# Optimization experiments

Measured on AMD Instinct MI355X. Metric: run time of the kernel, lower is better.

Reference implementation:

```python
import jax, jax.numpy as jnp
import numpy as np

D_MODEL = 1024
D_STATE = 16
EXPAND = 2
D_HEAD = 64
D_CONV = 4
FFN = 2816
NORMALIZE_BC = True
D_INNER = EXPAND * D_MODEL          # 2048
N_HEADS = D_INNER // D_HEAD         # 32
EPS = 1e-6


def _rmsnorm(x, w):
    v = jnp.mean(x * x, axis=-1, keepdims=True)
    return x * jax.lax.rsqrt(v + EPS) * w


def _mixer(x, in_proj_w, conv_w, conv_b, A_log, dt_bias, D, out_proj_w):
    b, l, _ = x.shape
    zxbcdt = x @ in_proj_w.T  # (b, l, 2*D_INNER + 2*D_STATE + N_HEADS)
    z, xBC, dt_raw = jnp.split(zxbcdt, [D_INNER, 2 * D_INNER + 2 * D_STATE], axis=-1)
    # causal depthwise conv over (u, B, C) channels
    xp = jnp.pad(xBC, ((0, 0), (D_CONV - 1, 0), (0, 0)))
    y = conv_b + sum(xp[:, k:k + l, :] * conv_w[:, k] for k in range(D_CONV))
    xBC = jax.nn.silu(y)
    u, Bm, Cm = jnp.split(xBC, [D_INNER, D_INNER + D_STATE], axis=-1)
    if NORMALIZE_BC:
        Bm = Bm / (jnp.linalg.norm(Bm, axis=-1, keepdims=True) + EPS)
        Cm = Cm / (jnp.linalg.norm(Cm, axis=-1, keepdims=True) + EPS)
    dt = jax.nn.softplus(dt_raw + dt_bias)          # (b, l, h)
    A = jnp.exp(A_log)                              # (h, n) oscillator frequencies >= 0
    u = u.reshape(b, l, N_HEADS, D_HEAD)

    # LinOSS implicit (IM) discretization of z' = -A y + B u ; y' = z
    #   S  = 1/(1 + dt^2 A)
    #   w_k = S*(w_{k-1} - dt*A*y_{k-1} + dt*B u_k)
    #   y_k = y_{k-1} + dt*w_k ;  out_k = C y_k + D u_k
    def step(carry, inp):
        w, ys = carry                               # each (b, h, dh, n)
        dt_t, B_t, C_t, u_t = inp                   # (b,h),(b,n),(b,n),(b,h,dh)
        S = 1.0 / (1.0 + (dt_t[:, :, None] ** 2) * A[None])   # (b,h,n)
        Sb = S[:, :, None, :]
        dtb = dt_t[:, :, None, None]
        Ab = A[None, :, None, :]
        Bu = B_t[:, None, None, :] * u_t[..., None]            # (b,h,dh,n)
        w = Sb * (w - dtb * Ab * ys + dtb * Bu)
        ys = ys + dtb * w
        o = jnp.einsum('bhdn,bn->bhd', ys, C_t)
        return (w, ys), o

    init = (jnp.zeros((b, N_HEADS, D_HEAD, D_STATE), x.dtype),
            jnp.zeros((b, N_HEADS, D_HEAD, D_STATE), x.dtype))
    xs = (dt.transpose(1, 0, 2), Bm.transpose(1, 0, 2),
          Cm.transpose(1, 0, 2), u.transpose(1, 0, 2, 3))
    _, ys = jax.lax.scan(step, init, xs)            # (l, b, h, dh)
    ys = ys.transpose(1, 0, 2, 3) + D[None, None, :, None] * u
    out = ys.reshape(b, l, D_INNER) * jax.nn.silu(z)
    return out @ out_proj_w.T


def setup_inputs() -> dict:
    key = jax.random.key(0)
    ks = jax.random.split(key, 12)
    B, L = 4, 2048
    proj_dim = 2 * D_INNER + 2 * D_STATE + N_HEADS
    conv_ch = D_INNER + 2 * D_STATE
    s = lambda k, shape, sc: jax.random.normal(k, shape, jnp.float32) * sc
    return {
        "x": s(ks[0], (B, L, D_MODEL), 1.0),
        "norm1_w": jnp.ones((D_MODEL,), jnp.float32),
        "in_proj_w": s(ks[1], (proj_dim, D_MODEL), D_MODEL ** -0.5),
        "conv_w": s(ks[2], (conv_ch, D_CONV), 0.3),
        "conv_b": jnp.zeros((conv_ch,), jnp.float32),
        "A_log": s(ks[3], (N_HEADS, D_STATE), 0.5),
        "dt_bias": s(ks[4], (N_HEADS,), 0.5),
        "D": s(ks[5], (N_HEADS,), 1.0),
        "out_proj_w": s(ks[6], (D_MODEL, D_INNER), D_INNER ** -0.5),
        "norm2_w": jnp.ones((D_MODEL,), jnp.float32),
        "gate_w": s(ks[7], (FFN, D_MODEL), D_MODEL ** -0.5),
        "up_w": s(ks[8], (FFN, D_MODEL), D_MODEL ** -0.5),
        "down_w": s(ks[9], (D_MODEL, FFN), FFN ** -0.5),
    }


def reference(x, norm1_w, in_proj_w, conv_w, conv_b, A_log, dt_bias, D,
              out_proj_w, norm2_w, gate_w, up_w, down_w):
    h = x + _mixer(_rmsnorm(x, norm1_w), in_proj_w, conv_w, conv_b,
                   A_log, dt_bias, D, out_proj_w)
    hn = _rmsnorm(h, norm2_w)
    ffn = (jax.nn.silu(hn @ gate_w.T) * (hn @ up_w.T)) @ down_w.T
    return h + ffn
```

## Files before the change

kernel.cpp:

```cpp
#include <hip/hip_runtime.h>
#include <hip/hip_bf16.h>

#define D_MODEL   1024
#define D_STATE   16
#define D_HEAD    64
#define D_CONV    4
#define FFN_DIM   2816
#define D_INNER   2048
#define N_HEADS   32
#define BATCH     4
#define SEQ       2048
#define ROWS      (BATCH*SEQ)
#define PROJ_DIM  4160
#define PROJ_PAD  4352
#define CONV_CH   2080
#define CH        128
#define NCH       (SEQ/CH)

typedef __bf16 bf16x8 __attribute__((ext_vector_type(8)));
typedef float  f32x4  __attribute__((ext_vector_type(4)));
typedef float  f32x2  __attribute__((ext_vector_type(2)));

__device__ __forceinline__ float siluf(float x) { return x / (1.0f + __expf(-x)); }

#define SBAR() do { asm volatile("" ::: "memory"); __builtin_amdgcn_s_barrier(); asm volatile("" ::: "memory"); } while (0)
#define LGKM0() asm volatile("s_waitcnt lgkmcnt(0)" ::: "memory")
#define VMCNT4() asm volatile("s_waitcnt vmcnt(4)" ::: "memory")
#define VMCNT2() asm volatile("s_waitcnt vmcnt(2)" ::: "memory")
#define VMCNT0() asm volatile("s_waitcnt vmcnt(0)" ::: "memory")

__global__ void cvt_k(const float* __restrict__ src, __hip_bfloat16* __restrict__ dst, int n) {
  int i = blockIdx.x * blockDim.x + threadIdx.x;
  if (i < n) dst[i] = __float2bfloat16(src[i]);
}

__global__ void cvt_pad_k(const float* __restrict__ src, __hip_bfloat16* __restrict__ dst) {
  int i = blockIdx.x * blockDim.x + threadIdx.x;
  if (i >= PROJ_PAD * D_MODEL) return;
  int row = i >> 10;
  dst[i] = (row < PROJ_DIM) ? __float2bfloat16(src[i]) : __float2bfloat16(0.0f);
}

__global__ __launch_bounds__(256) void rmsnorm_k(const float* __restrict__ x,
                                                 const float* __restrict__ w,
                                                 __hip_bfloat16* __restrict__ out,
                                                 float* __restrict__ outf) {
  int row = blockIdx.x;
  int t = threadIdx.x;
  const float* xr = x + (size_t)row * D_MODEL;
  float4 v = ((const float4*)xr)[t];
  float ss = v.x*v.x + v.y*v.y + v.z*v.z + v.w*v.w;
  #pragma unroll
  for (int o = 32; o > 0; o >>= 1) ss += __shfl_xor(ss, o);
  __shared__ float red[4];
  if ((t & 63) == 0) red[t >> 6] = ss;
  __syncthreads();
  ss = red[0] + red[1] + red[2] + red[3];
  float scale = rsqrtf(ss * (1.0f / D_MODEL) + 1e-6f);
  float4 wv = ((const float4*)w)[t];
  float4 r;
  r.x = v.x * scale * wv.x; r.y = v.y * scale * wv.y;
  r.z = v.z * scale * wv.z; r.w = v.w * scale * wv.w;
  __hip_bfloat16* orow = out + (size_t)row * D_MODEL + t * 4;
  orow[0] = __float2bfloat16(r.x);
  orow[1] = __float2bfloat16(r.y);
  orow[2] = __float2bfloat16(r.z);
  orow[3] = __float2bfloat16(r.w);
  if (outf) ((float4*)(outf + (size_t)row * D_MODEL))[t] = r;
}

__global__ __launch_bounds__(256) void dtproj_k(const float* __restrict__ xn,
                                                const float* __restrict__ wi,
                                                const float* __restrict__ dtb,
                                                float* __restrict__ dtT) {
  const int r0 = blockIdx.x * 4;
  const int t  = threadIdx.x;
  const int hh  = t >> 3;
  const int seg = t & 7;

  __shared__ float xs[4][D_MODEL];
  #pragma unroll
  for (int i = 0; i < 4; ++i)
    ((float4*)&xs[i][0])[t] = ((const float4*)(xn + (size_t)(r0 + i) * D_MODEL))[t];
  __syncthreads();

  const float4* w4 = (const float4*)(wi + (size_t)(2 * D_INNER + 2 * D_STATE + hh) * D_MODEL) + seg * 32;
  const float4* x0 = (const float4*)&xs[0][0] + seg * 32;
  const float4* x1 = (const float4*)&xs[1][0] + seg * 32;
  const float4* x2 = (const float4*)&xs[2][0] + seg * 32;
  const float4* x3 = (const float4*)&xs[3][0] + seg * 32;
  float a0 = 0.f, a1 = 0.f, a2 = 0.f, a3 = 0.f;
  #pragma unroll 8
  for (int k = 0; k < 32; ++k) {
    float4 wv = w4[k];
    float4 v0 = x0[k], v1 = x1[k], v2 = x2[k], v3 = x3[k];
    a0 = fmaf(wv.x, v0.x, fmaf(wv.y, v0.y, fmaf(wv.z, v0.z, fmaf(wv.w, v0.w, a0))));
    a1 = fmaf(wv.x, v1.x, fmaf(wv.y, v1.y, fmaf(wv.z, v1.z, fmaf(wv.w, v1.w, a1))));
    a2 = fmaf(wv.x, v2.x, fmaf(wv.y, v2.y, fmaf(wv.z, v2.z, fmaf(wv.w, v2.w, a2))));
    a3 = fmaf(wv.x, v3.x, fmaf(wv.y, v3.y, fmaf(wv.z, v3.z, fmaf(wv.w, v3.w, a3))));
  }
  #pragma unroll
  for (int m = 1; m < 8; m <<= 1) {
    a0 += __shfl_xor(a0, m);
    a1 += __shfl_xor(a1, m);
    a2 += __shfl_xor(a2, m);
    a3 += __shfl_xor(a3, m);
  }
  if (seg == 0) {
    float bias = dtb[hh];
    float v[4] = {a0, a1, a2, a3};
    #pragma unroll
    for (int i = 0; i < 4; ++i) {
      float xv = v[i] + bias;
      dtT[(size_t)hh * ROWS + r0 + i] = (xv > 20.f) ? xv : log1pf(__expf(xv));
    }
  }
}

template<int EPI>
__global__ __launch_bounds__(512, 2) void gemm8(
    const __hip_bfloat16* __restrict__ A,
    const __hip_bfloat16* __restrict__ Bw,
    float* __restrict__ Cf,
    __hip_bfloat16* __restrict__ Cb,
    const float* __restrict__ add_src,
    int M, int N, int K)
{
  extern __shared__ char lds[];
  const int nwg = (M >> 8) * (N >> 8);
  int bid = blockIdx.x;
  bid = (bid & 7) * (nwg >> 3) + (bid >> 3);
  const int ntn = N >> 8;
  const int bm = (bid / ntn) << 8;
  const int bn = (bid % ntn) << 8;

  const int tid  = threadIdx.x;
  const int wid  = tid >> 6;
  const int lane = tid & 63;
  const int wm = wid >> 2;
  const int wn = wid & 3;
  const int r16 = lane & 15;
  const int kg  = lane >> 4;

  const int rb = ((r16 << 6) + (kg << 4)) ^ ((r16 & 8) << 2);

  const int s_sub = tid >> 6;
  const int s_w   = (tid & 63) << 4;
  const int s_wp  = s_w ^ ((((s_w) >> 9) & 1) << 5);
  const int s_row = ((s_sub >> 1) << 4) + (s_wp >> 6);
  const int s_col = ((s_sub & 1) << 5) + ((s_wp >> 1) & 31);

  auto stage = [&](int buf, int mat, int half, int c, int kt) {
    const __hip_bfloat16* src = (mat == 0)
        ? A  + (size_t)(bm + half * 128 + c * 64 + s_row) * K + kt * 64 + s_col
        : Bw + (size_t)(bn + half * 128 + c * 64 + s_row) * K + kt * 64 + s_col;
    char* dst = lds + buf * 65536 + mat * 32768 + half * 16384 + c * 8192 + tid * 16;
    __builtin_amdgcn_global_load_lds((const __attribute__((address_space(1))) unsigned int*)src,
                                     (__attribute__((address_space(3))) unsigned int*)dst,
                                     16, 0, 0);
  };

  f32x4 acc[8][4] = {};
  bf16x8 af[4][2], bfr[4][2];

  const int NT = K >> 6;
  stage(0,0,0,0,0); stage(0,0,0,1,0); stage(0,0,1,0,0); stage(0,0,1,1,0);
  stage(0,1,0,0,0); stage(0,1,0,1,0); stage(0,1,1,0,0); stage(0,1,1,1,0);
  __syncthreads();

  for (int kt = 0; kt < NT; ++kt) {
    const int buf = kt & 1, nbuf = buf ^ 1;
    const bool st = (kt + 1 < NT);
    const char* Ab = lds + buf * 65536 + wm * 16384;
    const char* Bb = lds + buf * 65536 + 32768 + (wn >> 1) * 16384 + (wn & 1) * 8192;

    #pragma unroll
    for (int mi2 = 0; mi2 < 4; ++mi2)
      #pragma unroll
      for (int kk = 0; kk < 2; ++kk)
        af[mi2][kk] = *(const bf16x8*)(Ab + (mi2 * 2 + kk) * 1024 + rb);
    #pragma unroll
    for (int ni = 0; ni < 2; ++ni)
      #pragma unroll
      for (int kk = 0; kk < 2; ++kk)
        bfr[ni][kk] = *(const bf16x8*)(Bb + (ni * 2 + kk) * 1024 + rb);
    if (st) { stage(nbuf,1,0,0,kt+1); stage(nbuf,1,0,1,kt+1); }
    SBAR(); LGKM0();
    __builtin_amdgcn_s_setprio(1);
    #pragma unroll
    for (int mi2 = 0; mi2 < 4; ++mi2)
      #pragma unroll
      for (int ni = 0; ni < 2; ++ni)
        #pragma unroll
        for (int kk = 0; kk < 2; ++kk)
          acc[mi2][ni] = __builtin_amdgcn_mfma_f32_16x16x32_bf16(af[mi2][kk], bfr[ni][kk], acc[mi2][ni], 0, 0, 0);
    __builtin_amdgcn_s_setprio(0);
    SBAR();

    #pragma unroll
    for (int ni = 2; ni < 4; ++ni)
      #pragma unroll
      for (int kk = 0; kk < 2; ++kk)
        bfr[ni][kk] = *(const bf16x8*)(Bb + (ni * 2 + kk) * 1024 + rb);
    if (st) { stage(nbuf,1,1,0,kt+1); stage(nbuf,1,1,1,kt+1); }
    SBAR(); LGKM0();
    __builtin_amdgcn_s_setprio(1);
    #pragma unroll
    for (int mi2 = 0; mi2 < 4; ++mi2)
      #pragma unroll
      for (int ni = 2; ni < 4; ++ni)
        #pragma unroll
        for (int kk = 0; kk < 2; ++kk)
          acc[mi2][ni] = __builtin_amdgcn_mfma_f32_16x16x32_bf16(af[mi2][kk], bfr[ni][kk], acc[mi2][ni], 0, 0, 0);
    __builtin_amdgcn_s_setprio(0);
    if (st) { VMCNT4(); } else { VMCNT0(); }
    SBAR();

    #pragma unroll
    for (int mi2 = 0; mi2 < 4; ++mi2)
      #pragma unroll
      for (int kk = 0; kk < 2; ++kk)
        af[mi2][kk] = *(const bf16x8*)(Ab + ((4 + mi2) * 2 + kk) * 1024 + rb);
    if (st) { stage(nbuf,0,0,0,kt+1); stage(nbuf,0,1,0,kt+1); }
    SBAR(); LGKM0();
    __builtin_amdgcn_s_setprio(1);
    #pragma unroll
    for (int mi2 = 0; mi2 < 4; ++mi2)
      #pragma unroll
      for (int ni = 0; ni < 2; ++ni)
        #pragma unroll
        for (int kk = 0; kk < 2; ++kk)
          acc[4 + mi2][ni] = __builtin_amdgcn_mfma_f32_16x16x32_bf16(af[mi2][kk], bfr[ni][kk], acc[4 + mi2][ni], 0, 0, 0);
    __builtin_amdgcn_s_setprio(0);
    SBAR();

    if (st) { stage(nbuf,0,0,1,kt+1); stage(nbuf,0,1,1,kt+1); }
    SBAR(); LGKM0();
    __builtin_amdgcn_s_setprio(1);
    #pragma unroll
    for (int mi2 = 0; mi2 < 4; ++mi2)
      #pragma unroll
      for (int ni = 2; ni < 4; ++ni)
        #pragma unroll
        for (int kk = 0; kk < 2; ++kk)
          acc[4 + mi2][ni] = __builtin_amdgcn_mfma_f32_16x16x32_bf16(af[mi2][kk], bfr[ni][kk], acc[4 + mi2][ni], 0, 0, 0);
    __builtin_amdgcn_s_setprio(0);
    VMCNT2();
    SBAR();
  }

  #pragma unroll
  for (int mi = 0; mi < 8; ++mi) {
    #pragma unroll
    for (int ni = 0; ni < 4; ++ni) {
      #pragma unroll
      for (int j = 0; j < 4; ++j) {
        int r = bm + wm * 128 + mi * 16 + kg * 4 + j;
        int c = bn + wn * 64 + ni * 16 + r16;
        size_t idx = (size_t)r * N + c;
        float v = acc[mi][ni][j];
        if constexpr (EPI == 0) {
          Cf[idx] = v;
        } else if constexpr (EPI == 1) {
          Cf[idx] = v + add_src[idx];
        } else if constexpr (EPI == 2) {
          Cb[idx] = __float2bfloat16(siluf(v));
        } else if constexpr (EPI == 3) {
          Cb[idx] = __float2bfloat16(v * __bfloat162float(Cb[idx]));
        }
      }
    }
  }
}

template<int EPI>
__global__ __launch_bounds__(512, 2) void gemm8B(
    const __hip_bfloat16* __restrict__ A,
    const __hip_bfloat16* __restrict__ Bw,
    float* __restrict__ Cf,
    __hip_bfloat16* __restrict__ Cb,
    const float* __restrict__ add_src,
    int M, int N, int K)
{
  extern __shared__ char lds[];
  const int nwg = (M >> 8) * (N >> 7);
  int bid = blockIdx.x;
  bid = (bid & 7) * (nwg >> 3) + (bid >> 3);
  const int ntn = N >> 7;
  const int bm = (bid / ntn) << 8;
  const int bn = (bid % ntn) << 7;

  const int tid  = threadIdx.x;
  const int wid  = tid >> 6;
  const int lane = tid & 63;
  const int wm = wid >> 2;
  const int wn = wid & 3;
  const int r16 = lane & 15;
  const int kg  = lane >> 4;

  const int rb = ((r16 << 6) + (kg << 4)) ^ ((r16 & 8) << 2);

  const int s_sub = tid >> 6;
  const int s_w   = (tid & 63) << 4;
  const int s_wp  = s_w ^ ((((s_w) >> 9) & 1) << 5);
  const int s_row = ((s_sub >> 1) << 4) + (s_wp >> 6);
  const int s_col = ((s_sub & 1) << 5) + ((s_wp >> 1) & 31);

  auto stageA = [&](int buf, int half, int c, int kt) {
    const __hip_bfloat16* src = A + (size_t)(bm + half * 128 + c * 64 + s_row) * K + kt * 64 + s_col;
    char* dst = lds + buf * 65536 + half * 16384 + c * 8192 + tid * 16;
    __builtin_amdgcn_global_load_lds((const __attribute__((address_space(1))) unsigned int*)src,
                                     (__attribute__((address_space(3))) unsigned int*)dst,
                                     16, 0, 0);
  };
  auto stageB = [&](int buf, int c, int kt) {
    const __hip_bfloat16* src = Bw + (size_t)(bn + c * 64 + s_row) * K + kt * 64 + s_col;
    char* dst = lds + buf * 65536 + 32768 + c * 8192 + tid * 16;
    __builtin_amdgcn_global_load_lds((const __attribute__((address_space(1))) unsigned int*)src,
                                     (__attribute__((address_space(3))) unsigned int*)dst,
                                     16, 0, 0);
  };

  f32x4 acc[8][2] = {};
  bf16x8 af[4][2], bfr[2][2];

  const int NT = K >> 6;
  stageB(0,0,0); stageB(0,1,0);
  stageA(0,0,0,0); stageA(0,1,0,0); stageA(0,0,1,0); stageA(0,1,1,0);
  __syncthreads();

  for (int kt = 0; kt < NT; ++kt) {
    const int buf = kt & 1, nbuf = buf ^ 1;
    const bool st = (kt + 1 < NT);
    const char* Ab = lds + buf * 65536 + wm * 16384;
    const char* Bb = lds + buf * 65536 + 32768 + (wn >> 1) * 8192 + (wn & 1) * 4096;

    #pragma unroll
    for (int mi2 = 0; mi2 < 4; ++mi2)
      #pragma unroll
      for (int kk = 0; kk < 2; ++kk)
        af[mi2][kk] = *(const bf16x8*)(Ab + (mi2 * 2 + kk) * 1024 + rb);
    #pragma unroll
    for (int ni = 0; ni < 2; ++ni)
      #pragma unroll
      for (int kk = 0; kk < 2; ++kk)
        bfr[ni][kk] = *(const bf16x8*)(Bb + (ni * 2 + kk) * 1024 + rb);
    if (st) { stageB(nbuf,0,kt+1); stageB(nbuf,1,kt+1); stageA(nbuf,0,0,kt+1); stageA(nbuf,1,0,kt+1); }
    SBAR(); LGKM0();
    __builtin_amdgcn_s_setprio(1);
    #pragma unroll
    for (int mi2 = 0; mi2 < 4; ++mi2)
      #pragma unroll
      for (int ni = 0; ni < 2; ++ni)
        #pragma unroll
        for (int kk = 0; kk < 2; ++kk)
          acc[mi2][ni] = __builtin_amdgcn_mfma_f32_16x16x32_bf16(af[mi2][kk], bfr[ni][kk], acc[mi2][ni], 0, 0, 0);
    __builtin_amdgcn_s_setprio(0);
    if (st) { VMCNT4(); } else { VMCNT0(); }
    SBAR();

    #pragma unroll
    for (int mi2 = 0; mi2 < 4; ++mi2)
      #pragma unroll
      for (int kk = 0; kk < 2; ++kk)
        af[mi2][kk] = *(const bf16x8*)(Ab + ((4 + mi2) * 2 + kk) * 1024 + rb);
    if (st) { stageA(nbuf,0,1,kt+1); stageA(nbuf,1,1,kt+1); }
    SBAR(); LGKM0();
    __builtin_amdgcn_s_setprio(1);
    #pragma unroll
    for (int mi2 = 0; mi2 < 4; ++mi2)
      #pragma unroll
      for (int ni = 0; ni < 2; ++ni)
        #pragma unroll
        for (int kk = 0; kk < 2; ++kk)
          acc[4 + mi2][ni] = __builtin_amdgcn_mfma_f32_16x16x32_bf16(af[mi2][kk], bfr[ni][kk], acc[4 + mi2][ni], 0, 0, 0);
    __builtin_amdgcn_s_setprio(0);
    VMCNT2();
    SBAR();
  }

  #pragma unroll
  for (int mi = 0; mi < 8; ++mi) {
    #pragma unroll
    for (int ni = 0; ni < 2; ++ni) {
      #pragma unroll
      for (int j = 0; j < 4; ++j) {
        int r = bm + wm * 128 + mi * 16 + kg * 4 + j;
        int c = bn + wn * 32 + ni * 16 + r16;
        size_t idx = (size_t)r * N + c;
        float v = acc[mi][ni][j];
        if constexpr (EPI == 0) {
          Cf[idx] = v;
        } else if constexpr (EPI == 1) {
          Cf[idx] = v + add_src[idx];
        } else if constexpr (EPI == 2) {
          Cb[idx] = __float2bfloat16(siluf(v));
        } else if constexpr (EPI == 3) {
          Cb[idx] = __float2bfloat16(v * __bfloat162float(Cb[idx]));
        }
      }
    }
  }
}

__global__ __launch_bounds__(256) void duconv_k(const float* __restrict__ zx,
                                                const float* __restrict__ cw,
                                                const float* __restrict__ cb,
                                                __hip_bfloat16* __restrict__ u_po) {
  int idx = blockIdx.x * 256 + threadIdx.x;
  int q = idx & 511;
  int r = idx >> 9;
  int d0 = q << 2;
  int l = r & (SEQ - 1);
  float4 cb4 = ((const float4*)cb)[q];
  float tw[4][4];
  #pragma unroll
  for (int i = 0; i < 4; ++i) {
    float4 t = ((const float4*)cw)[d0 + i];
    tw[i][0] = t.x; tw[i][1] = t.y; tw[i][2] = t.z; tw[i][3] = t.w;
  }
  float a[4] = {cb4.x, cb4.y, cb4.z, cb4.w};
  #pragma unroll
  for (int k = 0; k < 4; ++k) {
    if (l - 3 + k >= 0) {
      float4 xv = *(const float4*)(zx + (size_t)(r - 3 + k) * PROJ_PAD + D_INNER + d0);
      a[0] = fmaf(xv.x, tw[0][k], a[0]);
      a[1] = fmaf(xv.y, tw[1][k], a[1]);
      a[2] = fmaf(xv.z, tw[2][k], a[2]);
      a[3] = fmaf(xv.w, tw[3][k], a[3]);
    }
  }
  union { ushort4 u4; __hip_bfloat16 b[4]; } pk;
  #pragma unroll
  for (int i = 0; i < 4; ++i) pk.b[i] = __float2bfloat16(siluf(a[i]));
  *(ushort4*)(u_po + (size_t)r * D_INNER + d0) = pk.u4;
}

__global__ __launch_bounds__(256) void bcdt_k(const float* __restrict__ zx,
                                              const float* __restrict__ cw,
                                              const float* __restrict__ cb,
                                              float* __restrict__ bc) {
  int t = threadIdx.x;
  int r = blockIdx.x * 8 + (t >> 5);
  int ch = t & 31;
  int l = r & (SEQ - 1);
  int c = D_INNER + ch;
  float acc = cb[c];
  #pragma unroll
  for (int k = 0; k < 4; ++k) {
    int lp = l - 3 + k;
    if (lp >= 0)
      acc = fmaf(zx[(size_t)(r - 3 + k) * PROJ_PAD + 2 * D_INNER + ch], cw[c * 4 + k], acc);
  }
  acc = siluf(acc);
  float ss = acc * acc;
  ss += __shfl_xor(ss, 1);
  ss += __shfl_xor(ss, 2);
  ss += __shfl_xor(ss, 4);
  ss += __shfl_xor(ss, 8);
  bc[r * 32 + ch] = acc / (sqrtf(ss) + 1e-6f);
}

__global__ __launch_bounds__(256) void pk_k(const float* __restrict__ dtT,
                                            const float* __restrict__ A_log,
                                            float* __restrict__ Pm) {
  int bh = blockIdx.x;
  int h = bh & 31;
  int t = threadIdx.x;
  int ch = t >> 4, n = t & 15;
  float a = __expf(A_log[h * 16 + n]);
  const float* dtp = dtT + (size_t)h * ROWS + (size_t)(bh >> 5) * SEQ + ch * CH;
  float p00 = 1.f, p01 = 0.f, p10 = 0.f, p11 = 1.f;
  for (int l = 0; l < CH; ++l) {
    float dt = dtp[l];
    float s  = 1.0f / fmaf(dt * dt, a, 1.0f);
    float m00 = s;
    float m01 = -dt * a * s;
    float m10 = dt * s;
    float m11 = fmaf(-dt * a, m10, 1.0f);
    float q00 = fmaf(m00, p00, m01 * p10);
    float q01 = fmaf(m00, p01, m01 * p11);
    float q10 = fmaf(m10, p00, m11 * p10);
    float q11 = fmaf(m10, p01, m11 * p11);
    p00 = q00; p01 = q01; p10 = q10; p11 = q11;
  }
  float4 v = {p00, p01, p10, p11};
  *(float4*)&Pm[(((size_t)bh * NCH + ch) * 16 + n) * 4] = v;
}

__global__ __launch_bounds__(256) void prop_k(const float* __restrict__ Pm,
                                              const float* __restrict__ pend,
                                              float* __restrict__ sinit) {
  int gid = blockIdx.x * 256 + threadIdx.x;
  int n  = gid & 15;
  int d  = (gid >> 4) & 63;
  int bh = gid >> 10;
  float s0 = 0.f, s1 = 0.f;
  for (int c = 0; c < NCH; ++c) {
    size_t i2 = (((size_t)bh * NCH + c) * 64 + d) * 16 + n;
    *(float2*)&sinit[i2 * 2] = make_float2(s0, s1);
    float4 P  = *(const float4*)&Pm[(((size_t)bh * NCH + c) * 16 + n) * 4];
    float2 pe = *(const float2*)&pend[i2 * 2];
    float t0 = fmaf(P.x, s0, fmaf(P.y, s1, pe.x));
    float t1 = fmaf(P.z, s0, fmaf(P.w, s1, pe.y));
    s0 = t0; s1 = t1;
  }
}

#define T_TILE 16
#define TPC (CH / T_TILE)
template<int PHASE>
__global__ __launch_bounds__(128) void scan_k(
    const float* __restrict__ zx, const float* __restrict__ bcb,
    const float* __restrict__ dtT, const float* __restrict__ A_log,
    const float* __restrict__ Dp, float* __restrict__ states,
    __hip_bfloat16* u_po)
{
  const int blk  = blockIdx.x;
  const int half = blk & 1;
  const int ch   = (blk >> 1) & 15;
  const int h    = (blk >> 5) & 31;
  const int b    = blk >> 10;
  const int bh   = b * 32 + h;
  const int tid  = threadIdx.x;
  const int wv   = tid >> 6;
  const int lane = tid & 63;
  const int d16  = lane & 15;
  const int ng   = lane >> 4;
  const int n0   = ng * 4;
  const int dwv  = wv * 16 + d16;
  const int dl   = half * 32 + dwv;
  const int dbase = h * 64 + half * 32;
  const size_t rowbase = (size_t)b * SEQ + (size_t)ch * CH;

  __shared__ __hip_bfloat16 dut[2][T_TILE][32];
  __shared__ float Btl[2][T_TILE][16];
  __shared__ float Ctl[PHASE == 3 ? 2 : 1][T_TILE][16];
  __shared__ float zt [PHASE == 3 ? 2 : 1][T_TILE][32];
  __shared__ float st [2][T_TILE][16];
  __shared__ float dtt[2][T_TILE];
  __shared__ float aexp[16];
  __shared__ float opart[PHASE == 3 ? T_TILE : 1][32][4];

  if (tid < 16) aexp[tid] = __expf(A_log[h * 16 + tid]);

  f32x2 A2[2];
  #pragma unroll
  for (int k = 0; k < 2; ++k) {
    A2[k][0] = __expf(A_log[h * 16 + n0 + 2 * k]);
    A2[k][1] = __expf(A_log[h * 16 + n0 + 2 * k + 1]);
  }
  const float Dh = Dp[h];

  auto stage = [&](int tile, int buf) {
    const size_t r0 = rowbase + (size_t)tile * T_TILE;
    if constexpr (PHASE == 3) {
      {
        int row = wv * 8 + (lane >> 3);
        const float* g = zx + (r0 + row) * PROJ_PAD + dbase + (lane & 7) * 4;
        float* l_ = &zt[buf][0][0] + wv * 256 + lane * 4;
        __builtin_amdgcn_global_load_lds((const __attribute__((address_space(1))) unsigned int*)g,
                                         (__attribute__((address_space(3))) unsigned int*)l_, 16, 0, 0);
      }
      if (wv == 0) {
        const __hip_bfloat16* g = u_po + (r0 + (lane >> 2)) * D_INNER + dbase + (lane & 3) * 8;
        __hip_bfloat16* l_ = &dut[buf][0][0] + lane * 8;
        __builtin_amdgcn_global_load_lds((const __attribute__((address_space(1))) unsigned int*)g,
                                         (__attribute__((address_space(3))) unsigned int*)l_, 16, 0, 0);
      } else {
        const float* gB = bcb + (r0 + (lane >> 2)) * 32 + (lane & 3) * 4;
        float* lB = &Btl[buf][0][0] + lane * 4;
        __builtin_amdgcn_global_load_lds((const __attribute__((address_space(1))) unsigned int*)gB,
                                         (__attribute__((address_space(3))) unsigned int*)lB, 16, 0, 0);
        const float* gC = bcb + (r0 + (lane >> 2)) * 32 + 16 + (lane & 3) * 4;
        float* lC = &Ctl[buf][0][0] + lane * 4;
        __builtin_amdgcn_global_load_lds((const __attribute__((address_space(1))) unsigned int*)gC,
                                         (__attribute__((address_space(3))) unsigned int*)lC, 16, 0, 0);
      }
    } else {
      if (wv == 0) {
        const __hip_bfloat16* g = u_po + (r0 + (lane >> 2)) * D_INNER + dbase + (lane & 3) * 8;
        __hip_bfloat16* l_ = &dut[buf][0][0] + lane * 8;
        __builtin_amdgcn_global_load_lds((const __attribute__((address_space(1))) unsigned int*)g,
                                         (__attribute__((address_space(3))) unsigned int*)l_, 16, 0, 0);
      } else {
        const float* gB = bcb + (r0 + (lane >> 2)) * 32 + (lane & 3) * 4;
        float* lB = &Btl[buf][0][0] + lane * 4;
        __builtin_amdgcn_global_load_lds((const __attribute__((address_space(1))) unsigned int*)gB,
                                         (__attribute__((address_space(3))) unsigned int*)lB, 16, 0, 0);
      }
    }
  };

  auto sprep = [&](int buf, float dtn) {
    #pragma unroll
    for (int i = 0; i < 2; ++i) {
      int idx = tid + 128 * i;
      int row = idx >> 4, n = idx & 15;
      float dv = __shfl(dtn, row);
      float a  = aexp[n];
      st[buf][row][n] = 1.0f / fmaf(dv * dv, a, 1.0f);
    }
  };

  stage(0, 0);
  float dtn = 0.f;
  if (lane < 16) dtn = dtT[(size_t)h * ROWS + rowbase + lane];
  __syncthreads();
  if (tid < 16) dtt[0][tid] = dtn;
  sprep(0, dtn);
  __syncthreads();

  f32x2 w2[2], ys2[2];
  if constexpr (PHASE == 1) {
    #pragma unroll
    for (int k = 0; k < 2; ++k) { w2[k] = (f32x2){0.f, 0.f}; ys2[k] = (f32x2){0.f, 0.f}; }
  } else {
    #pragma unroll
    for (int k = 0; k < 2; ++k)
      #pragma unroll
      for (int j = 0; j < 2; ++j) {
        size_t i2 = (((size_t)bh * NCH + ch) * 64 + dl) * 16 + (n0 + 2 * k + j);
        float2 s = *(const float2*)&states[i2 * 2];
        w2[k][j] = s.x; ys2[k][j] = s.y;
      }
  }
  int cur = 0;

  for (int t = 0; t < TPC; ++t) {
    if (t + 1 < TPC) {
      stage(t + 1, cur ^ 1);
      if (lane < 16) dtn = dtT[(size_t)h * ROWS + rowbase + (size_t)(t + 1) * T_TILE + lane];
    }
    #pragma unroll 4
    for (int l = 0; l < T_TILE; ++l) {
      float uv  = __bfloat162float(dut[cur][l][dwv]);
      float dtv = dtt[cur][l];
      f32x4 Sv4 = *(const f32x4*)&st [cur][l][n0];
      f32x4 Bv4 = *(const f32x4*)&Btl[cur][l][n0];
      float du = dtv * uv;
      f32x2 S2[2] = { {Sv4[0], Sv4[1]}, {Sv4[2], Sv4[3]} };
      f32x2 B2[2] = { {Bv4[0], Bv4[1]}, {Bv4[2], Bv4[3]} };
      if constexpr (PHASE == 3) {
        f32x4 Cv4 = *(const f32x4*)&Ctl[cur][l][n0];
        f32x2 C2[2] = { {Cv4[0], Cv4[1]}, {Cv4[2], Cv4[3]} };
        f32x2 o2 = {0.f, 0.f};
        #pragma unroll
        for (int k = 0; k < 2; ++k) {
          f32x2 dtA = dtv * A2[k];
          f32x2 tmp = w2[k] - dtA * ys2[k];
          tmp = tmp + du * B2[k];
          w2[k] = S2[k] * tmp;
          ys2[k] = ys2[k] + dtv * w2[k];
          o2 = o2 + ys2[k] * C2[k];
        }
        float o = o2[0] + o2[1];
        float ofin = (ng == 0) ? fmaf(Dh, uv, o) : o;
        opart[l][dwv][ng] = ofin;
      } else {
        #pragma unroll
        for (int k = 0; k < 2; ++k) {
          f32x2 dtA = dtv * A2[k];
          f32x2 tmp = w2[k] - dtA * ys2[k];
          tmp = tmp + du * B2[k];
          w2[k] = S2[k] * tmp;
          ys2[k] = ys2[k] + dtv * w2[k];
        }
      }
    }
    if constexpr (PHASE == 3) {
      #pragma unroll
      for (int i = 0; i < 4; ++i) {
        int l  = (lane >> 4) + 4 * i;
        int dd = wv * 16 + d16;
        f32x4 op = *(const f32x4*)&opart[l][dd][0];
        float zv = zt[cur][l][dd];
        float yv = (op[0] + op[1]) + (op[2] + op[3]);
        u_po[(rowbase + (size_t)t * T_TILE + l) * D_INNER + dbase + dd] =
            __float2bfloat16(yv * siluf(zv));
      }
    }
    __syncthreads();
    if (t + 1 < TPC) {
      if (tid < 16) dtt[cur ^ 1][tid] = dtn;
      sprep(cur ^ 1, dtn);
      __syncthreads();
    }
    cur ^= 1;
  }

  if constexpr (PHASE == 1) {
    #pragma unroll
    for (int k = 0; k < 2; ++k)
      #pragma unroll
      for (int j = 0; j < 2; ++j) {
        size_t i2 = (((size_t)bh * NCH + ch) * 64 + dl) * 16 + (n0 + 2 * k + j);
        *(float2*)&states[i2 * 2] = make_float2(w2[k][j], ys2[k][j]);
      }
  }
}

extern "C" void kernel_launch(void* const* d_in, const int* in_sizes, int n_in,
                              void* d_out, int out_size, void* d_ws, size_t ws_size,
                              hipStream_t stream) {
  const float* x     = (const float*)d_in[0];
  const float* n1w   = (const float*)d_in[1];
  const float* wi    = (const float*)d_in[2];
  const float* cw    = (const float*)d_in[3];
  const float* cb    = (const float*)d_in[4];
  const float* A_log = (const float*)d_in[5];
  const float* dtb   = (const float*)d_in[6];
  const float* Dp    = (const float*)d_in[7];
  const float* wo    = (const float*)d_in[8];
  const float* n2w   = (const float*)d_in[9];
  const float* wg    = (const float*)d_in[10];
  const float* wu    = (const float*)d_in[11];
  const float* wd    = (const float*)d_in[12];
  float* out = (float*)d_out;

  char* p = (char*)d_ws;
  auto take = [&](size_t b) { char* q = p; p += (b + 255) & ~(size_t)255; return q; };
  __hip_bfloat16* wbi  = (__hip_bfloat16*)take((size_t)PROJ_PAD * D_MODEL * 2);
  __hip_bfloat16* wbo  = (__hip_bfloat16*)take((size_t)D_MODEL * D_INNER * 2);
  __hip_bfloat16* wbg  = (__hip_bfloat16*)take((size_t)FFN_DIM * D_MODEL * 2);
  __hip_bfloat16* wbu  = (__hip_bfloat16*)take((size_t)FFN_DIM * D_MODEL * 2);
  __hip_bfloat16* wbd  = (__hip_bfloat16*)take((size_t)D_MODEL * FFN_DIM * 2);
  __hip_bfloat16* h0b  = (__hip_bfloat16*)take((size_t)ROWS * D_MODEL * 2);
  float*          zx   = (float*)take((size_t)ROWS * PROJ_PAD * 4);
  float*          bcb  = (float*)take((size_t)ROWS * 32 * 4);
  float*          dtT  = (float*)take((size_t)ROWS * 32 * 4);
  __hip_bfloat16* po   = (__hip_bfloat16*)take((size_t)ROWS * D_INNER * 2);
  float*          pend = (float*)take((size_t)128 * NCH * 64 * 16 * 2 * 4);
  float*          sini = (float*)take((size_t)128 * NCH * 64 * 16 * 2 * 4);
  float*          Pm   = (float*)take((size_t)128 * NCH * 16 * 4 * 4);
  float*          h0f  = (float*)zx;
  float*          h    = (float*)zx;
  __hip_bfloat16* gact = (__hip_bfloat16*)((char*)zx + 33554432);

  hipFuncSetAttribute(reinterpret_cast<const void*>(&gemm8<0>),  hipFuncAttributeMaxDynamicSharedMemorySize, 131072);
  hipFuncSetAttribute(reinterpret_cast<const void*>(&gemm8<2>),  hipFuncAttributeMaxDynamicSharedMemorySize, 131072);
  hipFuncSetAttribute(reinterpret_cast<const void*>(&gemm8<3>),  hipFuncAttributeMaxDynamicSharedMemorySize, 131072);
  hipFuncSetAttribute(reinterpret_cast<const void*>(&gemm8B<1>), hipFuncAttributeMaxDynamicSharedMemorySize, 131072);

  cvt_pad_k<<<(PROJ_PAD * D_MODEL + 255) / 256, 256, 0, stream>>>(wi, wbi);
  cvt_k<<<(D_MODEL * D_INNER + 255) / 256, 256, 0, stream>>>(wo, wbo, D_MODEL * D_INNER);
  cvt_k<<<(FFN_DIM * D_MODEL + 255) / 256, 256, 0, stream>>>(wg, wbg, FFN_DIM * D_MODEL);
  cvt_k<<<(FFN_DIM * D_MODEL + 255) / 256, 256, 0, stream>>>(wu, wbu, FFN_DIM * D_MODEL);
  cvt_k<<<(FFN_DIM * D_MODEL + 255) / 256, 256, 0, stream>>>(wd, wbd, FFN_DIM * D_MODEL);

  rmsnorm_k<<<ROWS, 256, 0, stream>>>(x, n1w, h0b, h0f);
  dtproj_k<<<ROWS / 4, 256, 0, stream>>>(h0f, wi, dtb, dtT);
  gemm8<0><<<(ROWS / 256) * (PROJ_PAD / 256), 512, 131072, stream>>>(h0b, wbi, zx, nullptr, nullptr,
                                                                     ROWS, PROJ_PAD, D_MODEL);
  duconv_k<<<ROWS * 512 / 256, 256, 0, stream>>>(zx, cw, cb, po);
  bcdt_k<<<ROWS / 8, 256, 0, stream>>>(zx, cw, cb, bcb);
  pk_k<<<BATCH * N_HEADS, 256, 0, stream>>>(dtT, A_log, Pm);
  scan_k<1><<<BATCH * N_HEADS * NCH * 2, 128, 0, stream>>>(zx, bcb, dtT, A_log, Dp, pend, po);
  prop_k<<<BATCH * N_HEADS * 64 * 16 / 256, 256, 0, stream>>>(Pm, pend, sini);
  scan_k<3><<<BATCH * N_HEADS * NCH * 2, 128, 0, stream>>>(zx, bcb, dtT, A_log, Dp, sini, po);
  gemm8B<1><<<(ROWS / 256) * (D_MODEL / 128), 512, 131072, stream>>>(po, wbo, h, nullptr, x,
                                                                     ROWS, D_MODEL, D_INNER);
  rmsnorm_k<<<ROWS, 256, 0, stream>>>(h, n2w, h0b, nullptr);
  gemm8<2><<<(ROWS / 256) * (FFN_DIM / 256), 512, 131072, stream>>>(h0b, wbg, nullptr, gact, nullptr,
                                                                    ROWS, FFN_DIM, D_MODEL);
  gemm8<3><<<(ROWS / 256) * (FFN_DIM / 256), 512, 131072, stream>>>(h0b, wbu, nullptr, gact, nullptr,
                                                                    ROWS, FFN_DIM, D_MODEL);
  gemm8B<1><<<(ROWS / 256) * (D_MODEL / 128), 512, 131072, stream>>>(gact, wbd, out, nullptr, h,
                                                                     ROWS, D_MODEL, FFN_DIM);
}
```

Baseline: 704.1 us.

## Fuse gate and up FFN GEMMs via interleaved weights and LDS exchange epilogue

Interleaves gate and up weight rows in 128-row blocks into one combined bf16 matrix so a single GEMM computes both projections per 256-wide tile. The epilogue writes silu(gate) to LDS and the up-half warps multiply by it, writing the bf16 product directly. This removes one GEMM launch, the intermediate bf16 write and read-back of the gate activation, and a second read of the normalized input. In exchange it adds an LDS round-trip with extra barriers in the epilogue, and only half the warps do the global stores.

```diff
diff --git a/kernel.cpp b/kernel.cpp
--- a/kernel.cpp
+++ b/kernel.cpp
@@ -16,6 +16,7 @@
 #define CONV_CH   2080
 #define CH        128
 #define NCH       (SEQ/CH)
+#define GU_N      5632
 
 typedef __bf16 bf16x8 __attribute__((ext_vector_type(8)));
 typedef float  f32x4  __attribute__((ext_vector_type(4)));
@@ -39,6 +40,18 @@
   if (i >= PROJ_PAD * D_MODEL) return;
   int row = i >> 10;
   dst[i] = (row < PROJ_DIM) ? __float2bfloat16(src[i]) : __float2bfloat16(0.0f);
+}
+
+__global__ void cvt_gu_k(const float* __restrict__ wg, const float* __restrict__ wu,
+                         __hip_bfloat16* __restrict__ dst) {
+  int i = blockIdx.x * blockDim.x + threadIdx.x;
+  if (i >= GU_N * D_MODEL) return;
+  int r = i >> 10, c = i & 1023;
+  int tile = r >> 8, rr = r & 255;
+  const float* src = (rr < 128)
+      ? wg + (size_t)(tile * 128 + rr) * D_MODEL + c
+      : wu + (size_t)(tile * 128 + (rr - 128)) * D_MODEL + c;
+  dst[i] = __float2bfloat16(*src);
 }
 
 __global__ __launch_bounds__(256) void rmsnorm_k(const float* __restrict__ x,
@@ -249,24 +262,55 @@
     SBAR();
   }
 
-  #pragma unroll
-  for (int mi = 0; mi < 8; ++mi) {
-    #pragma unroll
-    for (int ni = 0; ni < 4; ++ni) {
-      #pragma unroll
-      for (int j = 0; j < 4; ++j) {
-        int r = bm + wm * 128 + mi * 16 + kg * 4 + j;
-        int c = bn + wn * 64 + ni * 16 + r16;
-        size_t idx = (size_t)r * N + c;
-        float v = acc[mi][ni][j];
-        if constexpr (EPI == 0) {
-          Cf[idx] = v;
-        } else if constexpr (EPI == 1) {
-          Cf[idx] = v + add_src[idx];
-        } else if constexpr (EPI == 2) {
-          Cb[idx] = __float2bfloat16(siluf(v));
-        } else if constexpr (EPI == 3) {
-          Cb[idx] = __float2bfloat16(v * __bfloat162float(Cb[idx]));
+  if constexpr (EPI == 4) {
+    float* xch = (float*)lds;
+    __syncthreads();
+    if (wn < 2) {
+      #pragma unroll
+      for (int mi = 0; mi < 8; ++mi)
+        #pragma unroll
+        for (int ni = 0; ni < 4; ++ni)
+          #pragma unroll
+          for (int j = 0; j < 4; ++j) {
+            int row = mi * 16 + kg * 4 + j;
+            int col = wn * 64 + ni * 16 + r16;
+            int cc = col ^ (((row >> 2) & 1) << 4);
+            xch[wm * 16384 + row * 128 + cc] = siluf(acc[mi][ni][j]);
+          }
+    }
+    __syncthreads();
+    if (wn >= 2) {
+      #pragma unroll
+      for (int mi = 0; mi < 8; ++mi)
+        #pragma unroll
+        for (int ni = 0; ni < 4; ++ni)
+          #pragma unroll
+          for (int j = 0; j < 4; ++j) {
+            int row = mi * 16 + kg * 4 + j;
+            int col = (wn - 2) * 64 + ni * 16 + r16;
+            int cc = col ^ (((row >> 2) & 1) << 4);
+            float g = xch[wm * 16384 + row * 128 + cc];
+            int r = bm + wm * 128 + row;
+            int tc = (bn >> 1) + col;
+            Cb[(size_t)r * FFN_DIM + tc] = __float2bfloat16(g * acc[mi][ni][j]);
+          }
+    }
+  } else {
+    #pragma unroll
+    for (int mi = 0; mi < 8; ++mi) {
+      #pragma unroll
+      for (int ni = 0; ni < 4; ++ni) {
+        #pragma unroll
+        for (int j = 0; j < 4; ++j) {
+          int r = bm + wm * 128 + mi * 16 + kg * 4 + j;
+          int c = bn + wn * 64 + ni * 16 + r16;
+          size_t idx = (size_t)r * N + c;
+          float v = acc[mi][ni][j];
+          if constexpr (EPI == 0) {
+            Cf[idx] = v;
+          } else if constexpr (EPI == 1) {
+            Cf[idx] = v + add_src[idx];
+          }
         }
       }
     }
@@ -393,10 +437,6 @@
           Cf[idx] = v;
         } else if constexpr (EPI == 1) {
           Cf[idx] = v + add_src[idx];
-        } else if constexpr (EPI == 2) {
-          Cb[idx] = __float2bfloat16(siluf(v));
-        } else if constexpr (EPI == 3) {
-          Cb[idx] = __float2bfloat16(v * __bfloat162float(Cb[idx]));
         }
       }
     }
@@ -722,8 +762,7 @@
   auto take = [&](size_t b) { char* q = p; p += (b + 255) & ~(size_t)255; return q; };
   __hip_bfloat16* wbi  = (__hip_bfloat16*)take((size_t)PROJ_PAD * D_MODEL * 2);
   __hip_bfloat16* wbo  = (__hip_bfloat16*)take((size_t)D_MODEL * D_INNER * 2);
-  __hip_bfloat16* wbg  = (__hip_bfloat16*)take((size_t)FFN_DIM * D_MODEL * 2);
-  __hip_bfloat16* wbu  = (__hip_bfloat16*)take((size_t)FFN_DIM * D_MODEL * 2);
+  __hip_bfloat16* wgu  = (__hip_bfloat16*)take((size_t)GU_N * D_MODEL * 2);
   __hip_bfloat16* wbd  = (__hip_bfloat16*)take((size_t)D_MODEL * FFN_DIM * 2);
   __hip_bfloat16* h0b  = (__hip_bfloat16*)take((size_t)ROWS * D_MODEL * 2);
   float*          zx   = (float*)take((size_t)ROWS * PROJ_PAD * 4);
@@ -738,14 +777,12 @@
   __hip_bfloat16* gact = (__hip_bfloat16*)((char*)zx + 33554432);
 
   hipFuncSetAttribute(reinterpret_cast<const void*>(&gemm8<0>),  hipFuncAttributeMaxDynamicSharedMemorySize, 131072);
-  hipFuncSetAttribute(reinterpret_cast<const void*>(&gemm8<2>),  hipFuncAttributeMaxDynamicSharedMemorySize, 131072);
-  hipFuncSetAttribute(reinterpret_cast<const void*>(&gemm8<3>),  hipFuncAttributeMaxDynamicSharedMemorySize, 131072);
+  hipFuncSetAttribute(reinterpret_cast<const void*>(&gemm8<4>),  hipFuncAttributeMaxDynamicSharedMemorySize, 131072);
   hipFuncSetAttribute(reinterpret_cast<const void*>(&gemm8B<1>), hipFuncAttributeMaxDynamicSharedMemorySize, 131072);
 
   cvt_pad_k<<<(PROJ_PAD * D_MODEL + 255) / 256, 256, 0, stream>>>(wi, wbi);
   cvt_k<<<(D_MODEL * D_INNER + 255) / 256, 256, 0, stream>>>(wo, wbo, D_MODEL * D_INNER);
-  cvt_k<<<(FFN_DIM * D_MODEL + 255) / 256, 256, 0, stream>>>(wg, wbg, FFN_DIM * D_MODEL);
-  cvt_k<<<(FFN_DIM * D_MODEL + 255) / 256, 256, 0, stream>>>(wu, wbu, FFN_DIM * D_MODEL);
+  cvt_gu_k<<<(GU_N * D_MODEL + 255) / 256, 256, 0, stream>>>(wg, wu, wgu);
   cvt_k<<<(FFN_DIM * D_MODEL + 255) / 256, 256, 0, stream>>>(wd, wbd, FFN_DIM * D_MODEL);
 
   rmsnorm_k<<<ROWS, 256, 0, stream>>>(x, n1w, h0b, h0f);
@@ -761,10 +798,8 @@
   gemm8B<1><<<(ROWS / 256) * (D_MODEL / 128), 512, 131072, stream>>>(po, wbo, h, nullptr, x,
                                                                      ROWS, D_MODEL, D_INNER);
   rmsnorm_k<<<ROWS, 256, 0, stream>>>(h, n2w, h0b, nullptr);
-  gemm8<2><<<(ROWS / 256) * (FFN_DIM / 256), 512, 131072, stream>>>(h0b, wbg, nullptr, gact, nullptr,
-                                                                    ROWS, FFN_DIM, D_MODEL);
-  gemm8<3><<<(ROWS / 256) * (FFN_DIM / 256), 512, 131072, stream>>>(h0b, wbu, nullptr, gact, nullptr,
-                                                                    ROWS, FFN_DIM, D_MODEL);
+  gemm8<4><<<(ROWS / 256) * (GU_N / 256), 512, 131072, stream>>>(h0b, wgu, nullptr, gact, nullptr,
+                                                                 ROWS, GU_N, D_MODEL);
   gemm8B<1><<<(ROWS / 256) * (D_MODEL / 128), 512, 131072, stream>>>(gact, wbd, out, nullptr, h,
                                                                      ROWS, D_MODEL, FFN_DIM);
 }
```

After: 648.8 us. -7.8%, faster.
